# Optimization experiments

Hardware: AMD Instinct MI355X
Metric: run time of the kernel (lower is better)

Reference implementation:

```python
import jax, jax.numpy as jnp
import numpy as np

IN_DIM = 135909   # input feature vocab (Amazon-670K style)
OUT_DIM = 670091  # output classes
D = 128           # hardcoded embedding dim in the module
B = 256           # batch size
T = 100           # active features per sample (summed bag-of-features)


def setup_inputs() -> dict:
    key = jax.random.key(0)
    ks = jax.random.split(key, 6)
    x = jax.random.randint(ks[0], (B, T), 0, IN_DIM)
    y = jax.random.randint(ks[1], (B,), 0, OUT_DIM)
    # nn.Embedding(IN+1, 128, padding_idx=IN): last row is the zero padding row
    emb_table = jax.random.normal(ks[2], (IN_DIM + 1, D), jnp.float32) * 0.01
    emb_table = emb_table.at[IN_DIM].set(0.0)
    stdv = 1.0 / np.sqrt(IN_DIM)
    bias = jax.random.uniform(ks[3], (D,), jnp.float32, -stdv, stdv)
    # LSHSoftmax dense parameters: per-class weight [OUT, D] and bias [OUT]
    W = jax.random.normal(ks[4], (OUT_DIM, D), jnp.float32) * (1.0 / np.sqrt(D))
    b_out = jnp.zeros((OUT_DIM,), jnp.float32)
    return {"x": x, "y": y, "freeze": 0, "slide": 0,
            "emb_table": emb_table, "bias": bias, "W": W, "b_out": b_out}


def reference(x, y, freeze, slide, emb_table, bias, W, b_out):
    # raw_emb = sum over the feature indices (bag-of-features embedding sum)
    raw = jnp.sum(emb_table[x], axis=1)                      # [B, D]
    emb = raw / jnp.linalg.norm(raw, axis=1, keepdims=True)  # L2 normalize
    query = jax.nn.relu(emb + bias)                          # [B, D]
    # LSHSoftmax exact (slide=0 / full) path: dense softmax cross-entropy
    logits = query @ W.T + b_out                             # [B, OUT]
    logp = jax.nn.log_softmax(logits, axis=-1)
    loss = -jnp.mean(jnp.take_along_axis(logp, y[:, None], axis=1))
    return loss
```

## Files before the change

### kernel.cpp

```cpp
#include <hip/hip_runtime.h>
#include <hip/hip_bf16.h>

#define IN_DIMX 135909
#define OUT_DIMX 670091
#define DDIM 128
#define BATCH 256
#define TFEAT 100
#define NBLK 512
#define NCHUNK ((OUT_DIMX + 63) / 64)

typedef __bf16 bf16_t;
typedef __attribute__((ext_vector_type(4))) float f32x4;

__global__ void k_query(const int* __restrict__ x, const float* __restrict__ emb,
                        const float* __restrict__ bias, float* __restrict__ qf,
                        unsigned char* __restrict__ q8) {
    const int row = blockIdx.x;
    const int t = threadIdx.x;
    __shared__ int sidx[TFEAT];
    __shared__ float qs[DDIM];
    if (t < TFEAT) sidx[t] = x[row * TFEAT + t];
    __syncthreads();
    float s = 0.f;
    #pragma unroll 10
    for (int i = 0; i < TFEAT; ++i) {
        s += emb[(size_t)sidx[i] * DDIM + t];
    }
    float sq = s * s;
    #pragma unroll
    for (int off = 1; off < 64; off <<= 1) sq += __shfl_xor(sq, off, 64);
    __shared__ float wred[2];
    if ((t & 63) == 0) wred[t >> 6] = sq;
    __syncthreads();
    const float tot = wred[0] + wred[1];
    float q = s / sqrtf(tot) + bias[t];
    q = fmaxf(q, 0.f);
    qf[row * DDIM + t] = q;
    qs[t] = q;
    __syncthreads();
    if (t < 32) {
        int p = __builtin_amdgcn_cvt_pk_fp8_f32(qs[4 * t], qs[4 * t + 1], 0, false);
        p = __builtin_amdgcn_cvt_pk_fp8_f32(qs[4 * t + 2], qs[4 * t + 3], p, true);
        ((int*)q8)[row * 32 + t] = p;
    }
}

__global__ __launch_bounds__(256, 2)
void k_lse(const float* __restrict__ W, const float* __restrict__ b_out,
           const unsigned char* __restrict__ q8, float* __restrict__ partials) {
    __shared__ unsigned char lds[2][64 * DDIM];
    const int tid = threadIdx.x;
    const int lane = tid & 63;
    const int w = tid >> 6;
    const int l15 = lane & 15;
    const int l4 = lane >> 4;

    long a[4][4];
    #pragma unroll
    for (int mt = 0; mt < 4; ++mt)
        #pragma unroll
        for (int ks = 0; ks < 4; ++ks)
            a[mt][ks] = *(const long*)(q8 + (w * 64 + mt * 16 + l15) * DDIM + ks * 32 + 8 * l4);

    float rs[4][4];
    #pragma unroll
    for (int mt = 0; mt < 4; ++mt)
        #pragma unroll
        for (int r = 0; r < 4; ++r) rs[mt][r] = 0.f;

    const int srow = tid >> 5;
    const int scol4 = (tid & 31);
    const int c8 = scol4 >> 1;
    const int half = (scol4 & 1) * 4;

    f32x4 wr[8];
    float bo_n[4];

    auto issue = [&](int ch) {
        const int cb = ch * 64;
        #pragma unroll
        for (int j = 0; j < 8; ++j) {
            int r = cb + j * 8 + srow;
            r = (r < OUT_DIMX) ? r : 0;
            wr[j] = *(const f32x4*)(W + (size_t)r * DDIM + scol4 * 4);
        }
        #pragma unroll
        for (int nt = 0; nt < 4; ++nt) {
            int cc = cb + nt * 16 + l15;
            cc = (cc < OUT_DIMX) ? cc : 0;
            bo_n[nt] = b_out[cc];
        }
    };

    auto convwrite_reload = [&](int cur, bool has_next, int nch) {
        const int cb = nch * 64;
        #pragma unroll
        for (int j = 0; j < 8; ++j) {
            const int row = j * 8 + srow;
            const int sw = (c8 ^ (row & 7)) * 8 + half;
            int p = __builtin_amdgcn_cvt_pk_fp8_f32(wr[j][0], wr[j][1], 0, false);
            p = __builtin_amdgcn_cvt_pk_fp8_f32(wr[j][2], wr[j][3], p, true);
            *(int*)(&lds[cur][row * DDIM + sw]) = p;
            if (has_next) {
                int r = cb + j * 8 + srow;
                r = (r < OUT_DIMX) ? r : 0;
                wr[j] = *(const f32x4*)(W + (size_t)r * DDIM + scol4 * 4);
            }
        }
    };

    int cur = 0;
    issue(blockIdx.x);
    for (int ch = blockIdx.x; ch < NCHUNK; ch += NBLK) {
        float bo_c[4];
        #pragma unroll
        for (int nt = 0; nt < 4; ++nt) bo_c[nt] = bo_n[nt];

        const bool has_next = (ch + NBLK < NCHUNK);
        convwrite_reload(cur, has_next, has_next ? ch + NBLK : 0);
        if (has_next) {
            const int cb = (ch + NBLK) * 64;
            #pragma unroll
            for (int nt = 0; nt < 4; ++nt) {
                int cc = cb + nt * 16 + l15;
                cc = (cc < OUT_DIMX) ? cc : 0;
                bo_n[nt] = b_out[cc];
            }
        }
        asm volatile("s_waitcnt lgkmcnt(0)" ::: "memory");
        __builtin_amdgcn_s_barrier();
        asm volatile("" ::: "memory");

        f32x4 acc[4][4];
        #pragma unroll
        for (int mt = 0; mt < 4; ++mt)
            #pragma unroll
            for (int nt = 0; nt < 4; ++nt) acc[mt][nt] = (f32x4){0.f, 0.f, 0.f, 0.f};

        #pragma unroll
        for (int ks = 0; ks < 4; ++ks) {
            #pragma unroll
            for (int nt = 0; nt < 4; ++nt) {
                const int row = nt * 16 + l15;
                const int g = (ks * 4 + l4) ^ (row & 7);
                const long b = *(const long*)(&lds[cur][row * DDIM + g * 8]);
                #pragma unroll
                for (int mt = 0; mt < 4; ++mt)
                    acc[mt][nt] = __builtin_amdgcn_mfma_f32_16x16x32_fp8_fp8(
                        a[mt][ks], b, acc[mt][nt], 0, 0, 0);
            }
        }

        const int cbase = ch * 64;
        if (cbase + 64 <= OUT_DIMX) {
            #pragma unroll
            for (int nt = 0; nt < 4; ++nt)
                #pragma unroll
                for (int mt = 0; mt < 4; ++mt)
                    #pragma unroll
                    for (int r = 0; r < 4; ++r)
                        rs[mt][r] += __expf(acc[mt][nt][r] + bo_c[nt]);
        } else {
            #pragma unroll
            for (int nt = 0; nt < 4; ++nt) {
                const bool valid = (cbase + nt * 16 + l15 < OUT_DIMX);
                #pragma unroll
                for (int mt = 0; mt < 4; ++mt)
                    #pragma unroll
                    for (int r = 0; r < 4; ++r)
                        rs[mt][r] += valid ? __expf(acc[mt][nt][r] + bo_c[nt]) : 0.f;
            }
        }
        cur ^= 1;
    }

    #pragma unroll
    for (int mt = 0; mt < 4; ++mt)
        #pragma unroll
        for (int r = 0; r < 4; ++r) {
            float v = rs[mt][r];
            v += __shfl_xor(v, 1, 64);
            v += __shfl_xor(v, 2, 64);
            v += __shfl_xor(v, 4, 64);
            v += __shfl_xor(v, 8, 64);
            if (l15 == 0) {
                const int rowb = w * 64 + mt * 16 + l4 * 4 + r;
                partials[(size_t)rowb * NBLK + blockIdx.x] = v;
            }
        }
}

__global__ void k_rowlse(const float* __restrict__ partials,
                         const int* __restrict__ y,
                         const float* __restrict__ qf,
                         const float* __restrict__ W,
                         const float* __restrict__ b_out,
                         float* __restrict__ rowloss) {
    const int i = blockIdx.x;
    const int lane = threadIdx.x;
    float s = 0.f;
    #pragma unroll
    for (int k = 0; k < NBLK / 64; ++k)
        s += partials[(size_t)i * NBLK + k * 64 + lane];
    const int yi = y[i];
    const float* wrow = W + (size_t)yi * DDIM;
    const float* qrow = qf + i * DDIM;
    float d = qrow[lane] * wrow[lane] + qrow[lane + 64] * wrow[lane + 64];
    #pragma unroll
    for (int off = 1; off < 64; off <<= 1) {
        s += __shfl_xor(s, off, 64);
        d += __shfl_xor(d, off, 64);
    }
    if (lane == 0) rowloss[i] = logf(s) - (d + b_out[yi]);
}

__global__ void k_final(const float* __restrict__ rowloss, float* __restrict__ out) {
    const int i = threadIdx.x;
    float t = rowloss[i];
    #pragma unroll
    for (int off = 1; off < 64; off <<= 1) t += __shfl_xor(t, off, 64);
    __shared__ float wred[4];
    if ((threadIdx.x & 63) == 0) wred[threadIdx.x >> 6] = t;
    __syncthreads();
    if (threadIdx.x == 0)
        out[0] = (wred[0] + wred[1] + wred[2] + wred[3]) * (1.0f / (float)BATCH);
}

extern "C" void kernel_launch(void* const* d_in, const int* in_sizes, int n_in,
                              void* d_out, int out_size, void* d_ws, size_t ws_size,
                              hipStream_t stream) {
    const int*   x     = (const int*)d_in[0];
    const int*   y     = (const int*)d_in[1];
    const float* emb   = (const float*)d_in[4];
    const float* bias  = (const float*)d_in[5];
    const float* W     = (const float*)d_in[6];
    const float* b_out = (const float*)d_in[7];
    float* out = (float*)d_out;

    char* ws = (char*)d_ws;
    unsigned char* q8 = (unsigned char*)(ws);
    float*  qf       = (float*)(ws + 65536);
    float*  rowloss  = (float*)(ws + 197632);
    float*  partials = (float*)(ws + 262144);

    k_query<<<BATCH, DDIM, 0, stream>>>(x, emb, bias, qf, q8);
    k_lse<<<NBLK, 256, 0, stream>>>(W, b_out, q8, partials);
    k_rowlse<<<BATCH, 64, 0, stream>>>(partials, y, qf, W, b_out, rowloss);
    k_final<<<1, 256, 0, stream>>>(rowloss, out);
}
```

Before: 84.04 us.

## Pre-scale by log2e for exp2 and overlap next-chunk LDS fill with softmax

```diff
diff --git a/kernel.cpp b/kernel.cpp
--- a/kernel.cpp
+++ b/kernel.cpp
@@ -8,6 +8,7 @@
 #define TFEAT 100
 #define NBLK 512
 #define NCHUNK ((OUT_DIMX + 63) / 64)
+#define LOG2E 1.44269504088896f
 
 typedef __bf16 bf16_t;
 typedef __attribute__((ext_vector_type(4))) float f32x4;
@@ -36,7 +37,7 @@
     float q = s / sqrtf(tot) + bias[t];
     q = fmaxf(q, 0.f);
     qf[row * DDIM + t] = q;
-    qs[t] = q;
+    qs[t] = q * LOG2E;
     __syncthreads();
     if (t < 32) {
         int p = __builtin_amdgcn_cvt_pk_fp8_f32(qs[4 * t], qs[4 * t + 1], 0, false);
@@ -74,9 +75,9 @@
     const int half = (scol4 & 1) * 4;
 
     f32x4 wr[8];
-    float bo_n[4];
-
-    auto issue = [&](int ch) {
+    float bo_c[4], bo_n[4];
+
+    auto issue = [&](int ch, float (&bo)[4]) {
         const int cb = ch * 64;
         #pragma unroll
         for (int j = 0; j < 8; ++j) {
@@ -88,11 +89,11 @@
         for (int nt = 0; nt < 4; ++nt) {
             int cc = cb + nt * 16 + l15;
             cc = (cc < OUT_DIMX) ? cc : 0;
-            bo_n[nt] = b_out[cc];
+            bo[nt] = b_out[cc] * LOG2E;
         }
     };
 
-    auto convwrite_reload = [&](int cur, bool has_next, int nch) {
+    auto convwrite_reload = [&](int buf, bool do_reload, int nch) {
         const int cb = nch * 64;
         #pragma unroll
         for (int j = 0; j < 8; ++j) {
@@ -100,42 +101,42 @@
             const int sw = (c8 ^ (row & 7)) * 8 + half;
             int p = __builtin_amdgcn_cvt_pk_fp8_f32(wr[j][0], wr[j][1], 0, false);
             p = __builtin_amdgcn_cvt_pk_fp8_f32(wr[j][2], wr[j][3], p, true);
-            *(int*)(&lds[cur][row * DDIM + sw]) = p;
-            if (has_next) {
+            *(int*)(&lds[buf][row * DDIM + sw]) = p;
+            if (do_reload) {
                 int r = cb + j * 8 + srow;
                 r = (r < OUT_DIMX) ? r : 0;
                 wr[j] = *(const f32x4*)(W + (size_t)r * DDIM + scol4 * 4);
             }
         }
-    };
-
-    int cur = 0;
-    issue(blockIdx.x);
-    for (int ch = blockIdx.x; ch < NCHUNK; ch += NBLK) {
-        float bo_c[4];
-        #pragma unroll
-        for (int nt = 0; nt < 4; ++nt) bo_c[nt] = bo_n[nt];
-
-        const bool has_next = (ch + NBLK < NCHUNK);
-        convwrite_reload(cur, has_next, has_next ? ch + NBLK : 0);
-        if (has_next) {
-            const int cb = (ch + NBLK) * 64;
+        if (do_reload) {
             #pragma unroll
             for (int nt = 0; nt < 4; ++nt) {
                 int cc = cb + nt * 16 + l15;
                 cc = (cc < OUT_DIMX) ? cc : 0;
-                bo_n[nt] = b_out[cc];
-            }
-        }
-        asm volatile("s_waitcnt lgkmcnt(0)" ::: "memory");
-        __builtin_amdgcn_s_barrier();
-        asm volatile("" ::: "memory");
-
+                bo_n[nt] = b_out[cc] * LOG2E;
+            }
+        }
+    };
+
+    const int c0 = blockIdx.x;
+    issue(c0, bo_c);
+    convwrite_reload(0, false, 0);
+    {
+        const int c1 = c0 + NBLK;
+        issue(c1 < NCHUNK ? c1 : 0, bo_n);
+    }
+    asm volatile("s_waitcnt lgkmcnt(0)" ::: "memory");
+    __builtin_amdgcn_s_barrier();
+    asm volatile("" ::: "memory");
+
+    int cur = 0;
+    for (int ch = c0; ch < NCHUNK; ch += NBLK) {
         f32x4 acc[4][4];
         #pragma unroll
         for (int mt = 0; mt < 4; ++mt)
             #pragma unroll
-            for (int nt = 0; nt < 4; ++nt) acc[mt][nt] = (f32x4){0.f, 0.f, 0.f, 0.f};
+            for (int nt = 0; nt < 4; ++nt)
+                acc[mt][nt] = (f32x4){bo_c[nt], bo_c[nt], bo_c[nt], bo_c[nt]};
 
         #pragma unroll
         for (int ks = 0; ks < 4; ++ks) {
@@ -151,6 +152,14 @@
             }
         }
 
+        const bool has_next = (ch + NBLK < NCHUNK);
+        if (has_next) {
+            #pragma unroll
+            for (int nt = 0; nt < 4; ++nt) bo_c[nt] = bo_n[nt];
+            const int c2 = ch + 2 * NBLK;
+            convwrite_reload(cur ^ 1, c2 < NCHUNK, c2 < NCHUNK ? c2 : 0);
+        }
+
         const int cbase = ch * 64;
         if (cbase + 64 <= OUT_DIMX) {
             #pragma unroll
@@ -159,7 +168,7 @@
                 for (int mt = 0; mt < 4; ++mt)
                     #pragma unroll
                     for (int r = 0; r < 4; ++r)
-                        rs[mt][r] += __expf(acc[mt][nt][r] + bo_c[nt]);
+                        rs[mt][r] += __builtin_amdgcn_exp2f(acc[mt][nt][r]);
         } else {
             #pragma unroll
             for (int nt = 0; nt < 4; ++nt) {
@@ -168,9 +177,13 @@
                 for (int mt = 0; mt < 4; ++mt)
                     #pragma unroll
                     for (int r = 0; r < 4; ++r)
-                        rs[mt][r] += valid ? __expf(acc[mt][nt][r] + bo_c[nt]) : 0.f;
-            }
-        }
+                        rs[mt][r] += valid ? __builtin_amdgcn_exp2f(acc[mt][nt][r]) : 0.f;
+            }
+        }
+
+        asm volatile("s_waitcnt lgkmcnt(0)" ::: "memory");
+        __builtin_amdgcn_s_barrier();
+        asm volatile("" ::: "memory");
         cur ^= 1;
     }
 
```

Result: slower. 98.85 us (+17.6%).
